# Performance work log

Measured on AMD Instinct MI355X. Metric: run time of the kernel, lower is better.

Reference implementation:

```python
import jax, jax.numpy as jnp
import numpy as np

B, N, D, H = 32, 128, 64, 8
DH = D // H  # 8
LN_EPS = 1e-5


def _layer_norm(x, g, b):
    m = jnp.mean(x, axis=-1, keepdims=True)
    v = jnp.mean(jnp.square(x - m), axis=-1, keepdims=True)
    return (x - m) * jax.lax.rsqrt(v + LN_EPS) * g + b


def setup_inputs() -> dict:
    key = jax.random.key(0)
    ks = jax.random.split(key, 16)
    s = 0.05
    return {
        "h": jax.random.normal(ks[0], (B, N, D), jnp.float32),
        "p": jax.random.normal(ks[1], (B, N, D), jnp.float32),
        "e": jax.random.normal(ks[2], (B, N, N, D), jnp.float32),
        "k_RW": jax.random.uniform(ks[3], (B, N, N), jnp.float32),
        # projection weights stored as [in, out] (x @ W == torch Linear)
        "Wq": jax.random.normal(ks[4], (D, D), jnp.float32) * s,
        "Wk": jax.random.normal(ks[5], (D, D), jnp.float32) * s,
        "We": jax.random.normal(ks[6], (D, D), jnp.float32) * s,
        "Wv": jax.random.normal(ks[7], (D, D), jnp.float32) * s,
        "Wo": jax.random.normal(ks[8], (D, D), jnp.float32) * s,
        "bo": jnp.zeros((D,), jnp.float32),
        "ln1_g": jnp.ones((D,), jnp.float32),
        "ln1_b": jnp.zeros((D,), jnp.float32),
        "W1": jax.random.normal(ks[9], (D, 2 * D), jnp.float32) * s,
        "b1": jnp.zeros((2 * D,), jnp.float32),
        "W2": jax.random.normal(ks[10], (2 * D, D), jnp.float32) * s,
        "b2": jnp.zeros((D,), jnp.float32),
        "ln2_g": jnp.ones((D,), jnp.float32),
        "ln2_b": jnp.zeros((D,), jnp.float32),
    }


def reference(h, p, e, k_RW, Wq, Wk, We, Wv, Wo, bo, ln1_g, ln1_b, W1, b1, W2, b2, ln2_g, ln2_b):
    b, n, _ = h.shape
    Qh = (h @ Wq).reshape(b, n, H, DH)
    Kh = (h @ Wk).reshape(b, n, H, DH) * (DH ** -0.5)
    Vh = (h @ Wv).reshape(b, n, H, DH).transpose(0, 2, 1, 3)  # [b,h,n,d]
    E = (e @ We).reshape(b, n, n, H, DH)
    # edge-modulated scores: [b,h,i,j]
    scores = jnp.einsum('bihk,bjhk,bijhk->bhij', Qh, Kh, E)
    scores = jnp.exp(jnp.clip(scores, -5.0, 5.0))
    scores = scores * k_RW[:, None]  # adaptive edge PE scaling
    denom = jnp.maximum(scores.sum(-1, keepdims=True), 1e-6)
    attn = (scores @ Vh) / denom  # [b,h,n,d]
    attn = attn.transpose(0, 2, 1, 3).reshape(b, n, H * DH)
    h1 = h + (attn @ Wo + bo)  # residual + O projection
    h1 = _layer_norm(h1, ln1_g, ln1_b)
    ff = jax.nn.relu(h1 @ W1 + b1) @ W2 + b2
    h2 = _layer_norm(h1 + ff, ln2_g, ln2_b)
    return h2
```

## Files before the change

kernel.cpp:

```cpp
#include <hip/hip_runtime.h>


#define NB 32
#define NN 128
#define ND 64
#define G 4

typedef __attribute__((ext_vector_type(8))) __bf16 bf16x8;
typedef __attribute__((ext_vector_type(8))) unsigned short u16x8;
typedef __attribute__((ext_vector_type(4))) float f32x4;

static __device__ __forceinline__ unsigned short f2bf(float x) {
  unsigned u = __float_as_uint(x);
  u += 0x7fffu + ((u >> 16) & 1u);
  return (unsigned short)(u >> 16);
}
static __device__ __forceinline__ float bf2f(unsigned short u) {
  return __uint_as_float(((unsigned)u) << 16);
}

#define DPP_ADD(v, ctrl) \
  ((v) + __int_as_float(__builtin_amdgcn_update_dpp(0, __float_as_int(v), (ctrl), 0xf, 0xf, true)))

static __device__ __forceinline__ float wsum64(float v) {
  v += __shfl_xor(v, 1, 64);
  v += __shfl_xor(v, 2, 64);
  v += __shfl_xor(v, 4, 64);
  v += __shfl_xor(v, 8, 64);
  v += __shfl_xor(v, 16, 64);
  v += __shfl_xor(v, 32, 64);
  return v;
}

static __device__ __forceinline__ float4 xor_add4(float4 a, int m) {
  a.x += __shfl_xor(a.x, m, 64);
  a.y += __shfl_xor(a.y, m, 64);
  a.z += __shfl_xor(a.z, m, 64);
  a.w += __shfl_xor(a.w, m, 64);
  return a;
}

__global__ __launch_bounds__(64) void qkv_kernel(
    const float* __restrict__ h, const float* __restrict__ Wq,
    const float* __restrict__ Wk, const float* __restrict__ Wv,
    const float* __restrict__ We,
    float* __restrict__ Q, float* __restrict__ K, float* __restrict__ V,
    unsigned short* __restrict__ WeT) {
  if (blockIdx.x == NB * NN) {
    const int t = threadIdx.x;
#pragma unroll
    for (int k0 = 0; k0 < ND; k0 += 8) {
      u16x8 u;
#pragma unroll
      for (int j = 0; j < 8; ++j) u[j] = f2bf(We[(k0 + j) * ND + t]);
      *(u16x8*)(&WeT[t * ND + k0]) = u;
    }
    return;
  }
  const int r = blockIdx.x;
  const int t = threadIdx.x;
  __shared__ float hrow[ND];
  hrow[t] = h[(size_t)r * ND + t];
  __syncthreads();
  float q = 0.f, k = 0.f, v = 0.f;
#pragma unroll 8
  for (int d = 0; d < ND; ++d) {
    const float hv = hrow[d];
    q = fmaf(hv, Wq[d * ND + t], q);
    k = fmaf(hv, Wk[d * ND + t], k);
    v = fmaf(hv, Wv[d * ND + t], v);
  }
  Q[(size_t)r * ND + t] = q;
  K[(size_t)r * ND + t] = k * 0.35355339059327373f;
  V[(size_t)r * ND + t] = v;
}

__global__ __launch_bounds__(256, 4) void fused_kernel(
    const float* __restrict__ h, const float* __restrict__ e,
    const float* __restrict__ kRW,
    const float* __restrict__ Wo, const float* __restrict__ bo,
    const float* __restrict__ g1, const float* __restrict__ be1,
    const float* __restrict__ W1, const float* __restrict__ b1,
    const float* __restrict__ W2, const float* __restrict__ b2,
    const float* __restrict__ g2, const float* __restrict__ be2,
    const float* __restrict__ Q, const float* __restrict__ K,
    const float* __restrict__ V, const unsigned short* __restrict__ WeT,
    float* __restrict__ out) {
  const int blk = blockIdx.x;
  const int b = blk >> 5;
  const int i0 = (blk & 31) * G;
  const int tid = threadIdx.x;
  const int w = tid >> 6;
  const int L = tid & 63;
  const int quad = L >> 4;
  const int lrow = L & 15;

  __shared__ __align__(16) unsigned short e_lds[NN * 72];
  __shared__ __align__(16) unsigned short S_lds[G * 8 * 136];
  __shared__ float q_lds[G * ND];
  __shared__ float krw_lds[G * NN];
  __shared__ float attn_l[G * ND];
  __shared__ float n1_l[G * ND];
  __shared__ float ff_l[G * 2 * ND];

  const size_t row0 = (size_t)b * NN + i0;
  const size_t kvbase = (size_t)b * NN * ND;

  q_lds[tid] = Q[row0 * ND + tid];
  krw_lds[tid] = kRW[row0 * NN + tid];
  krw_lds[256 + tid] = kRW[row0 * NN + 256 + tid];

  bf16x8 bfr[2][4];
#pragma unroll
  for (int ks = 0; ks < 2; ++ks)
#pragma unroll
    for (int n0 = 0; n0 < 4; ++n0)
      bfr[ks][n0] = __builtin_bit_cast(
          bf16x8, *(const u16x8*)(&WeT[(n0 * 16 + lrow) * ND + ks * 32 + quad * 8]));

  float kreg[2][4][4];
#pragma unroll
  for (int mt = 0; mt < 2; ++mt)
#pragma unroll
    for (int n0 = 0; n0 < 4; ++n0)
#pragma unroll
      for (int reg = 0; reg < 4; ++reg)
        kreg[mt][n0][reg] =
            K[kvbase + (size_t)((w + mt * 4) * 16 + quad * 4 + reg) * ND + n0 * 16 + lrow];

  __syncthreads();

  for (int g = 0; g < G; ++g) {
    const float* ep = e + (row0 + g) * (size_t)(NN * ND);
#pragma unroll
    for (int p = 0; p < 8; ++p) {
      const int idx = p * 1024 + tid * 4;
      const float4 v = *(const float4*)(ep + idx);
      const int r = idx >> 6;
      const int c = idx & 63;
      *(ushort4*)(&e_lds[r * 72 + c]) =
          make_ushort4(f2bf(v.x), f2bf(v.y), f2bf(v.z), f2bf(v.w));
    }
    __syncthreads();
#pragma unroll
    for (int mt = 0; mt < 2; ++mt) {
      const int mr = w + mt * 4;
      bf16x8 afr[2];
#pragma unroll
      for (int ks = 0; ks < 2; ++ks)
        afr[ks] = __builtin_bit_cast(
            bf16x8, *(const u16x8*)(&e_lds[(mr * 16 + lrow) * 72 + ks * 32 + quad * 8]));
      f32x4 acc[4];
#pragma unroll
      for (int n0 = 0; n0 < 4; ++n0) acc[n0] = (f32x4){0.f, 0.f, 0.f, 0.f};
#pragma unroll
      for (int ks = 0; ks < 2; ++ks)
#pragma unroll
        for (int n0 = 0; n0 < 4; ++n0)
          acc[n0] =
              __builtin_amdgcn_mfma_f32_16x16x32_bf16(afr[ks], bfr[ks][n0], acc[n0], 0, 0, 0);

      const float4 krw4 = *(const float4*)(&krw_lds[g * NN + mr * 16 + quad * 4]);
      const float* krwp = (const float*)&krw4;
#pragma unroll
      for (int n0 = 0; n0 < 4; ++n0) {
        const float qn = q_lds[g * ND + n0 * 16 + lrow];
        float sv[4];
#pragma unroll
        for (int reg = 0; reg < 4; ++reg) {
          float tv = acc[n0][reg] * qn * kreg[mt][n0][reg];
          tv = DPP_ADD(tv, 0xB1);
          tv = DPP_ADD(tv, 0x4E);
          tv = DPP_ADD(tv, 0x141);
          sv[reg] = __expf(fminf(fmaxf(tv, -5.f), 5.f)) * krwp[reg];
        }
        if ((L & 7) == 0) {
          const int hh = n0 * 2 + ((L >> 3) & 1);
          *(ushort4*)(&S_lds[(g * 8 + hh) * 136 + mr * 16 + quad * 4]) =
              make_ushort4(f2bf(sv[0]), f2bf(sv[1]), f2bf(sv[2]), f2bf(sv[3]));
        }
      }
    }
    __syncthreads();
  }

  const size_t row = row0 + w;
  const int jj = L >> 4;
  const int c4 = L & 15;
  const int hh2 = c4 >> 1;

  float4 an = make_float4(0.f, 0.f, 0.f, 0.f);
  float den = 0.f;
#pragma unroll 8
  for (int t = 0; t < 32; ++t) {
    const int j = t * 4 + jj;
    const float s = bf2f(S_lds[(w * 8 + hh2) * 136 + j]);
    const float4 v = *(const float4*)(&V[kvbase + (size_t)j * ND + c4 * 4]);
    an.x = fmaf(s, v.x, an.x);
    an.y = fmaf(s, v.y, an.y);
    an.z = fmaf(s, v.z, an.z);
    an.w = fmaf(s, v.w, an.w);
    den += s;
  }
  an = xor_add4(an, 16); an = xor_add4(an, 32);
  den += __shfl_xor(den, 16, 64); den += __shfl_xor(den, 32, 64);
  const float rden = 1.f / fmaxf(den, 1e-6f);
  if (L < 16)
    *(float4*)(&attn_l[w * ND + c4 * 4]) =
        make_float4(an.x * rden, an.y * rden, an.z * rden, an.w * rden);
  __builtin_amdgcn_wave_barrier();

  float4 o4 = make_float4(0.f, 0.f, 0.f, 0.f);
#pragma unroll 4
  for (int t = 0; t < 16; ++t) {
    const int d = t * 4 + jj;
    const float a = attn_l[w * ND + d];
    const float4 wv = *(const float4*)(&Wo[d * ND + c4 * 4]);
    o4.x = fmaf(a, wv.x, o4.x);
    o4.y = fmaf(a, wv.y, o4.y);
    o4.z = fmaf(a, wv.z, o4.z);
    o4.w = fmaf(a, wv.w, o4.w);
  }
  o4 = xor_add4(o4, 16); o4 = xor_add4(o4, 32);
  const float4 bo4 = *(const float4*)(&bo[c4 * 4]);
  const float4 h4 = *(const float4*)(&h[row * ND + c4 * 4]);
  float4 h1;
  h1.x = h4.x + bo4.x + o4.x;
  h1.y = h4.y + bo4.y + o4.y;
  h1.z = h4.z + bo4.z + o4.z;
  h1.w = h4.w + bo4.w + o4.w;
  const float m1 = wsum64(h1.x + h1.y + h1.z + h1.w) * (1.f / 256.f);
  float4 df;
  df.x = h1.x - m1; df.y = h1.y - m1; df.z = h1.z - m1; df.w = h1.w - m1;
  const float v1 =
      wsum64(df.x * df.x + df.y * df.y + df.z * df.z + df.w * df.w) * (1.f / 256.f);
  const float r1 = rsqrtf(v1 + 1e-5f);
  const float4 g14 = *(const float4*)(&g1[c4 * 4]);
  const float4 be14 = *(const float4*)(&be1[c4 * 4]);
  float4 n14;
  n14.x = df.x * r1 * g14.x + be14.x;
  n14.y = df.y * r1 * g14.y + be14.y;
  n14.z = df.z * r1 * g14.z + be14.z;
  n14.w = df.w * r1 * g14.w + be14.w;
  if (L < 16) *(float4*)(&n1_l[w * ND + c4 * 4]) = n14;
  __builtin_amdgcn_wave_barrier();

  const int dd2 = L >> 5;
  const int c5 = L & 31;
  float4 f4 = make_float4(0.f, 0.f, 0.f, 0.f);
#pragma unroll 8
  for (int t = 0; t < 32; ++t) {
    const int d = t * 2 + dd2;
    const float nv = n1_l[w * ND + d];
    const float4 wv = *(const float4*)(&W1[d * 128 + c5 * 4]);
    f4.x = fmaf(nv, wv.x, f4.x);
    f4.y = fmaf(nv, wv.y, f4.y);
    f4.z = fmaf(nv, wv.z, f4.z);
    f4.w = fmaf(nv, wv.w, f4.w);
  }
  f4 = xor_add4(f4, 32);
  const float4 b14 = *(const float4*)(&b1[c5 * 4]);
  if (L < 32)
    *(float4*)(&ff_l[w * 2 * ND + c5 * 4]) =
        make_float4(fmaxf(f4.x + b14.x, 0.f), fmaxf(f4.y + b14.y, 0.f),
                    fmaxf(f4.z + b14.z, 0.f), fmaxf(f4.w + b14.w, 0.f));
  __builtin_amdgcn_wave_barrier();

  float4 q4 = make_float4(0.f, 0.f, 0.f, 0.f);
#pragma unroll 8
  for (int t = 0; t < 32; ++t) {
    const int u = t * 4 + jj;
    const float fv = ff_l[w * 2 * ND + u];
    const float4 wv = *(const float4*)(&W2[u * ND + c4 * 4]);
    q4.x = fmaf(fv, wv.x, q4.x);
    q4.y = fmaf(fv, wv.y, q4.y);
    q4.z = fmaf(fv, wv.z, q4.z);
    q4.w = fmaf(fv, wv.w, q4.w);
  }
  q4 = xor_add4(q4, 16); q4 = xor_add4(q4, 32);
  const float4 b24 = *(const float4*)(&b2[c4 * 4]);
  float4 x4;
  x4.x = n14.x + b24.x + q4.x;
  x4.y = n14.y + b24.y + q4.y;
  x4.z = n14.z + b24.z + q4.z;
  x4.w = n14.w + b24.w + q4.w;
  const float m2 = wsum64(x4.x + x4.y + x4.z + x4.w) * (1.f / 256.f);
  float4 d2;
  d2.x = x4.x - m2; d2.y = x4.y - m2; d2.z = x4.z - m2; d2.w = x4.w - m2;
  const float v2 =
      wsum64(d2.x * d2.x + d2.y * d2.y + d2.z * d2.z + d2.w * d2.w) * (1.f / 256.f);
  const float r2 = rsqrtf(v2 + 1e-5f);
  const float4 g24 = *(const float4*)(&g2[c4 * 4]);
  const float4 be24 = *(const float4*)(&be2[c4 * 4]);
  if (L < 16)
    *(float4*)(&out[row * ND + c4 * 4]) =
        make_float4(d2.x * r2 * g24.x + be24.x, d2.y * r2 * g24.y + be24.y,
                    d2.z * r2 * g24.z + be24.z, d2.w * r2 * g24.w + be24.w);
}

extern "C" void kernel_launch(void* const* d_in, const int* in_sizes, int n_in,
                              void* d_out, int out_size, void* d_ws, size_t ws_size,
                              hipStream_t stream) {
  const float* h   = (const float*)d_in[0];
  const float* e   = (const float*)d_in[2];
  const float* kRW = (const float*)d_in[3];
  const float* Wq  = (const float*)d_in[4];
  const float* Wk  = (const float*)d_in[5];
  const float* We  = (const float*)d_in[6];
  const float* Wv  = (const float*)d_in[7];
  const float* Wo  = (const float*)d_in[8];
  const float* bo  = (const float*)d_in[9];
  const float* g1  = (const float*)d_in[10];
  const float* be1 = (const float*)d_in[11];
  const float* W1  = (const float*)d_in[12];
  const float* b1  = (const float*)d_in[13];
  const float* W2  = (const float*)d_in[14];
  const float* b2  = (const float*)d_in[15];
  const float* g2  = (const float*)d_in[16];
  const float* be2 = (const float*)d_in[17];
  float* out = (float*)d_out;

  float* Q = (float*)d_ws;
  float* K = Q + (size_t)NB * NN * ND;
  float* V = K + (size_t)NB * NN * ND;
  unsigned short* WeT = (unsigned short*)(V + (size_t)NB * NN * ND);

  qkv_kernel<<<NB * NN + 1, 64, 0, stream>>>(h, Wq, Wk, Wv, We, Q, K, V, WeT);
  fused_kernel<<<NB * NN / G, 256, 0, stream>>>(h, e, kRW, Wo, bo, g1, be1,
                                                W1, b1, W2, b2, g2, be2, Q, K, V, WeT, out);
}
```

Measured before the change: 249.6 us.

## Split fused kernel into score and tail kernels; double-buffer edge tiles

```diff
diff --git a/kernel.cpp b/kernel.cpp
--- a/kernel.cpp
+++ b/kernel.cpp
@@ -75,17 +75,11 @@
   V[(size_t)r * ND + t] = v;
 }
 
-__global__ __launch_bounds__(256, 4) void fused_kernel(
-    const float* __restrict__ h, const float* __restrict__ e,
-    const float* __restrict__ kRW,
-    const float* __restrict__ Wo, const float* __restrict__ bo,
-    const float* __restrict__ g1, const float* __restrict__ be1,
-    const float* __restrict__ W1, const float* __restrict__ b1,
-    const float* __restrict__ W2, const float* __restrict__ b2,
-    const float* __restrict__ g2, const float* __restrict__ be2,
+__global__ __launch_bounds__(256, 4) void score_kernel(
+    const float* __restrict__ e, const float* __restrict__ kRW,
     const float* __restrict__ Q, const float* __restrict__ K,
-    const float* __restrict__ V, const unsigned short* __restrict__ WeT,
-    float* __restrict__ out) {
+    const unsigned short* __restrict__ WeT,
+    unsigned short* __restrict__ Sws) {
   const int blk = blockIdx.x;
   const int b = blk >> 5;
   const int i0 = (blk & 31) * G;
@@ -95,13 +89,9 @@
   const int quad = L >> 4;
   const int lrow = L & 15;
 
-  __shared__ __align__(16) unsigned short e_lds[NN * 72];
-  __shared__ __align__(16) unsigned short S_lds[G * 8 * 136];
+  __shared__ __align__(16) unsigned short e_lds[2][NN * 72];
   __shared__ float q_lds[G * ND];
   __shared__ float krw_lds[G * NN];
-  __shared__ float attn_l[G * ND];
-  __shared__ float n1_l[G * ND];
-  __shared__ float ff_l[G * 2 * ND];
 
   const size_t row0 = (size_t)b * NN + i0;
   const size_t kvbase = (size_t)b * NN * ND;
@@ -128,20 +118,27 @@
         kreg[mt][n0][reg] =
             K[kvbase + (size_t)((w + mt * 4) * 16 + quad * 4 + reg) * ND + n0 * 16 + lrow];
 
-  __syncthreads();
-
-  for (int g = 0; g < G; ++g) {
-    const float* ep = e + (row0 + g) * (size_t)(NN * ND);
+  float4 pf[8];
+  {
+    const float* ep = e + row0 * (size_t)(NN * ND);
+#pragma unroll
+    for (int p = 0; p < 8; ++p) pf[p] = *(const float4*)(ep + p * 1024 + tid * 4);
 #pragma unroll
     for (int p = 0; p < 8; ++p) {
       const int idx = p * 1024 + tid * 4;
-      const float4 v = *(const float4*)(ep + idx);
-      const int r = idx >> 6;
-      const int c = idx & 63;
-      *(ushort4*)(&e_lds[r * 72 + c]) =
-          make_ushort4(f2bf(v.x), f2bf(v.y), f2bf(v.z), f2bf(v.w));
-    }
-    __syncthreads();
+      *(ushort4*)(&e_lds[0][(idx >> 6) * 72 + (idx & 63)]) =
+          make_ushort4(f2bf(pf[p].x), f2bf(pf[p].y), f2bf(pf[p].z), f2bf(pf[p].w));
+    }
+  }
+  __syncthreads();
+
+  for (int g = 0; g < G; ++g) {
+    const int buf = g & 1;
+    if (g + 1 < G) {
+      const float* ep = e + (row0 + g + 1) * (size_t)(NN * ND);
+#pragma unroll
+      for (int p = 0; p < 8; ++p) pf[p] = *(const float4*)(ep + p * 1024 + tid * 4);
+    }
 #pragma unroll
     for (int mt = 0; mt < 2; ++mt) {
       const int mr = w + mt * 4;
@@ -149,7 +146,7 @@
 #pragma unroll
       for (int ks = 0; ks < 2; ++ks)
         afr[ks] = __builtin_bit_cast(
-            bf16x8, *(const u16x8*)(&e_lds[(mr * 16 + lrow) * 72 + ks * 32 + quad * 8]));
+            bf16x8, *(const u16x8*)(&e_lds[buf][(mr * 16 + lrow) * 72 + ks * 32 + quad * 8]));
       f32x4 acc[4];
 #pragma unroll
       for (int n0 = 0; n0 < 4; ++n0) acc[n0] = (f32x4){0.f, 0.f, 0.f, 0.f};
@@ -176,25 +173,50 @@
         }
         if ((L & 7) == 0) {
           const int hh = n0 * 2 + ((L >> 3) & 1);
-          *(ushort4*)(&S_lds[(g * 8 + hh) * 136 + mr * 16 + quad * 4]) =
+          *(ushort4*)(&Sws[((row0 + g) * 8 + hh) * NN + mr * 16 + quad * 4]) =
               make_ushort4(f2bf(sv[0]), f2bf(sv[1]), f2bf(sv[2]), f2bf(sv[3]));
         }
       }
     }
+    if (g + 1 < G) {
+#pragma unroll
+      for (int p = 0; p < 8; ++p) {
+        const int idx = p * 1024 + tid * 4;
+        *(ushort4*)(&e_lds[1 - buf][(idx >> 6) * 72 + (idx & 63)]) =
+            make_ushort4(f2bf(pf[p].x), f2bf(pf[p].y), f2bf(pf[p].z), f2bf(pf[p].w));
+      }
+    }
     __syncthreads();
   }
-
-  const size_t row = row0 + w;
+}
+
+__global__ __launch_bounds__(64) void tail_kernel(
+    const float* __restrict__ h, const unsigned short* __restrict__ Sws,
+    const float* __restrict__ V,
+    const float* __restrict__ Wo, const float* __restrict__ bo,
+    const float* __restrict__ g1, const float* __restrict__ be1,
+    const float* __restrict__ W1, const float* __restrict__ b1,
+    const float* __restrict__ W2, const float* __restrict__ b2,
+    const float* __restrict__ g2, const float* __restrict__ be2,
+    float* __restrict__ out) {
+  const int row = blockIdx.x;
+  const int b = row >> 7;
+  const int L = threadIdx.x;
   const int jj = L >> 4;
   const int c4 = L & 15;
   const int hh2 = c4 >> 1;
+  const size_t kvbase = (size_t)b * NN * ND;
+
+  __shared__ float attn_l[ND];
+  __shared__ float n1_l[ND];
+  __shared__ float ff_l[2 * ND];
 
   float4 an = make_float4(0.f, 0.f, 0.f, 0.f);
   float den = 0.f;
 #pragma unroll 8
   for (int t = 0; t < 32; ++t) {
     const int j = t * 4 + jj;
-    const float s = bf2f(S_lds[(w * 8 + hh2) * 136 + j]);
+    const float s = bf2f(Sws[((size_t)row * 8 + hh2) * NN + j]);
     const float4 v = *(const float4*)(&V[kvbase + (size_t)j * ND + c4 * 4]);
     an.x = fmaf(s, v.x, an.x);
     an.y = fmaf(s, v.y, an.y);
@@ -206,7 +228,7 @@
   den += __shfl_xor(den, 16, 64); den += __shfl_xor(den, 32, 64);
   const float rden = 1.f / fmaxf(den, 1e-6f);
   if (L < 16)
-    *(float4*)(&attn_l[w * ND + c4 * 4]) =
+    *(float4*)(&attn_l[c4 * 4]) =
         make_float4(an.x * rden, an.y * rden, an.z * rden, an.w * rden);
   __builtin_amdgcn_wave_barrier();
 
@@ -214,7 +236,7 @@
 #pragma unroll 4
   for (int t = 0; t < 16; ++t) {
     const int d = t * 4 + jj;
-    const float a = attn_l[w * ND + d];
+    const float a = attn_l[d];
     const float4 wv = *(const float4*)(&Wo[d * ND + c4 * 4]);
     o4.x = fmaf(a, wv.x, o4.x);
     o4.y = fmaf(a, wv.y, o4.y);
@@ -223,7 +245,7 @@
   }
   o4 = xor_add4(o4, 16); o4 = xor_add4(o4, 32);
   const float4 bo4 = *(const float4*)(&bo[c4 * 4]);
-  const float4 h4 = *(const float4*)(&h[row * ND + c4 * 4]);
+  const float4 h4 = *(const float4*)(&h[(size_t)row * ND + c4 * 4]);
   float4 h1;
   h1.x = h4.x + bo4.x + o4.x;
   h1.y = h4.y + bo4.y + o4.y;
@@ -242,7 +264,7 @@
   n14.y = df.y * r1 * g14.y + be14.y;
   n14.z = df.z * r1 * g14.z + be14.z;
   n14.w = df.w * r1 * g14.w + be14.w;
-  if (L < 16) *(float4*)(&n1_l[w * ND + c4 * 4]) = n14;
+  if (L < 16) *(float4*)(&n1_l[c4 * 4]) = n14;
   __builtin_amdgcn_wave_barrier();
 
   const int dd2 = L >> 5;
@@ -251,7 +273,7 @@
 #pragma unroll 8
   for (int t = 0; t < 32; ++t) {
     const int d = t * 2 + dd2;
-    const float nv = n1_l[w * ND + d];
+    const float nv = n1_l[d];
     const float4 wv = *(const float4*)(&W1[d * 128 + c5 * 4]);
     f4.x = fmaf(nv, wv.x, f4.x);
     f4.y = fmaf(nv, wv.y, f4.y);
@@ -261,7 +283,7 @@
   f4 = xor_add4(f4, 32);
   const float4 b14 = *(const float4*)(&b1[c5 * 4]);
   if (L < 32)
-    *(float4*)(&ff_l[w * 2 * ND + c5 * 4]) =
+    *(float4*)(&ff_l[c5 * 4]) =
         make_float4(fmaxf(f4.x + b14.x, 0.f), fmaxf(f4.y + b14.y, 0.f),
                     fmaxf(f4.z + b14.z, 0.f), fmaxf(f4.w + b14.w, 0.f));
   __builtin_amdgcn_wave_barrier();
@@ -270,7 +292,7 @@
 #pragma unroll 8
   for (int t = 0; t < 32; ++t) {
     const int u = t * 4 + jj;
-    const float fv = ff_l[w * 2 * ND + u];
+    const float fv = ff_l[u];
     const float4 wv = *(const float4*)(&W2[u * ND + c4 * 4]);
     q4.x = fmaf(fv, wv.x, q4.x);
     q4.y = fmaf(fv, wv.y, q4.y);
@@ -293,7 +315,7 @@
   const float4 g24 = *(const float4*)(&g2[c4 * 4]);
   const float4 be24 = *(const float4*)(&be2[c4 * 4]);
   if (L < 16)
-    *(float4*)(&out[row * ND + c4 * 4]) =
+    *(float4*)(&out[(size_t)row * ND + c4 * 4]) =
         make_float4(d2.x * r2 * g24.x + be24.x, d2.y * r2 * g24.y + be24.y,
                     d2.z * r2 * g24.z + be24.z, d2.w * r2 * g24.w + be24.w);
 }
@@ -324,8 +346,10 @@
   float* K = Q + (size_t)NB * NN * ND;
   float* V = K + (size_t)NB * NN * ND;
   unsigned short* WeT = (unsigned short*)(V + (size_t)NB * NN * ND);
+  unsigned short* Sws = WeT + (size_t)ND * ND;
 
   qkv_kernel<<<NB * NN + 1, 64, 0, stream>>>(h, Wq, Wk, Wv, We, Q, K, V, WeT);
-  fused_kernel<<<NB * NN / G, 256, 0, stream>>>(h, e, kRW, Wo, bo, g1, be1,
-                                                W1, b1, W2, b2, g2, be2, Q, K, V, WeT, out);
-}
+  score_kernel<<<NB * NN / G, 256, 0, stream>>>(e, kRW, Q, K, WeT, Sws);
+  tail_kernel<<<NB * NN, 64, 0, stream>>>(h, Sws, V, Wo, bo, g1, be1,
+                                          W1, b1, W2, b2, g2, be2, out);
+}
```

New measurement: 336.5 us. 1.35x slower.
